# Optimization experiments

Hardware: AMD Instinct MI355X
Metric: run time of the kernel (lower is better)

## Reference

```python
import jax, jax.numpy as jnp
import numpy as np

RELU_SCALE = 0.25  # const power-of-two activation scale for QuantReLU (uint4)
DN = ('NCHW', 'OIHW', 'NCHW')
BN_EPS = 1e-5


def ste_round(x):
    # straight-through-estimator round (brevitas RoundSte)
    return x + jax.lax.stop_gradient(jnp.round(x) - x)


def fq_signed(x, bits):
    # per-tensor symmetric fixed-point fake quant with power-of-two scale
    # (Int8WeightPerTensorFixedPoint / Int8ActPerTensorFixedPoint at bit_width=bits)
    n = 2.0 ** (bits - 1) - 1.0
    m = jnp.maximum(jnp.max(jnp.abs(x)), 1e-8)
    s = jax.lax.stop_gradient(jnp.exp2(jnp.ceil(jnp.log2(m / n))))
    return jnp.clip(ste_round(x / s), -n - 1.0, n) * s


def quant_relu4(x):
    # QuantReLU: uint4, CONST power-of-two scale
    return jnp.clip(ste_round(x / RELU_SCALE), 0.0, 15.0) * RELU_SCALE


def bn(x, g, b, m, v):
    # inference-form BatchNorm2d (running stats)
    inv = g * jax.lax.rsqrt(v + BN_EPS)
    return x * inv[None, :, None, None] + (b - m * inv)[None, :, None, None]


def qconv(x, w, stride, groups):
    # QuantConv2d: fake-quant input (int4) and weight (int4), then conv
    xq = fq_signed(x, 4)
    wq = fq_signed(w, 4)
    pad = 'VALID' if w.shape[-1] == 1 else ((1, 1), (1, 1))
    return jax.lax.conv_general_dilated(
        xq, wq, (stride, stride), pad,
        dimension_numbers=DN, feature_group_count=groups)


def setup_inputs() -> dict:
    key = jax.random.key(0)
    ks = jax.random.split(key, 24)
    B, Cin, H, W = 32, 64, 56, 56
    expansion, Cout = 6, 96
    P = expansion * Cin  # 384

    def bn_params(i, C):
        g = jax.random.uniform(ks[i], (C,), minval=0.5, maxval=1.5)
        b = jax.random.normal(ks[i + 1], (C,)) * 0.1
        m = jax.random.normal(ks[i + 2], (C,)) * 0.1
        v = jax.random.uniform(ks[i + 3], (C,), minval=0.5, maxval=1.5)
        return g, b, m, v

    x = jax.random.normal(ks[0], (B, Cin, H, W), dtype=jnp.float32)
    w1 = jax.random.normal(ks[1], (P, Cin, 1, 1), dtype=jnp.float32) * 0.1
    w2 = jax.random.normal(ks[2], (P, 1, 3, 3), dtype=jnp.float32) * 0.1
    w3 = jax.random.normal(ks[3], (Cout, P, 1, 1), dtype=jnp.float32) * 0.1
    ws = jax.random.normal(ks[4], (Cout, Cin, 1, 1), dtype=jnp.float32) * 0.1
    g1, b1, m1, v1 = bn_params(5, P)
    g2, b2, m2, v2 = bn_params(9, P)
    g3, b3, m3, v3 = bn_params(13, Cout)
    gs, bs, ms, vs = bn_params(17, Cout)
    return {
        'x': x,
        'w1': w1, 'g1': g1, 'b1': b1, 'm1': m1, 'v1': v1,
        'w2': w2, 'g2': g2, 'b2': b2, 'm2': m2, 'v2': v2,
        'w3': w3, 'g3': g3, 'b3': b3, 'm3': m3, 'v3': v3,
        'ws': ws, 'gs': gs, 'bs': bs, 'ms': ms, 'vs': vs,
    }


def reference(x, w1, g1, b1, m1, v1, w2, g2, b2, m2, v2,
              w3, g3, b3, m3, v3, ws, gs, bs, ms, vs):
    P = w1.shape[0]
    # expand 1x1 -> BN -> QuantReLU
    out = quant_relu4(bn(qconv(x, w1, 1, 1), g1, b1, m1, v1))
    # depthwise 3x3 (stride=1) -> BN -> QuantReLU
    out = quant_relu4(bn(qconv(out, w2, 1, P), g2, b2, m2, v2))
    # project 1x1 with int8 output_quant -> BN
    out = bn(fq_signed(qconv(out, w3, 1, 1), 8), g3, b3, m3, v3)
    # shortcut: 1x1 quant conv (int4 output_quant) -> BN  (stride==1, Cin!=Cout)
    sc = bn(fq_signed(qconv(x, ws, 1, 1), 4), gs, bs, ms, vs)
    return quant_relu4(out + sc)
```

## Files before the change

kernel.cpp:

```cpp
#include <hip/hip_runtime.h>
#include <stdint.h>

#define B_  32
#define CIN 64
#define H_  56
#define W_  56
#define HW_ 3136
#define P_  384
#define CO_ 96

typedef unsigned short u16;
typedef short v2s __attribute__((ext_vector_type(2)));

__device__ __forceinline__ v2s as_v2s(int x) {
    union { int i; v2s v; } u; u.i = x; return u.v;
}

__device__ __forceinline__ float pot_scale(float m, float n) {
    float q = fmaxf(m, 1e-8f) / n;
    int e; float f = frexpf(q, &e);
    return ldexpf(1.0f, (f == 0.5f) ? (e - 1) : e);
}

__device__ __forceinline__ int dot8(int a, int b, int c) {
#if __has_builtin(__builtin_amdgcn_sdot8)
    return __builtin_amdgcn_sdot8(a, b, c, false);
#else
#pragma unroll
    for (int j = 0; j < 8; j++) {
        int av = (a << (28 - 4 * j)) >> 28;
        int bv = (b << (28 - 4 * j)) >> 28;
        c += av * bv;
    }
    return c;
#endif
}

__device__ __forceinline__ int iclamp(int v, int lo, int hi) { return min(max(v, lo), hi); }

__device__ __forceinline__ unsigned build_lut(float r, int lo) {
    unsigned v = 0;
#pragma unroll
    for (int L = 0; L < 8; L++)
        v |= (unsigned)min((int)rintf(__fmul_rn((float)(lo + L), r)), 7) << (4 * L);
    return v;
}
__device__ __forceinline__ int lut1(unsigned lo, unsigned hi, int L) {
    unsigned sel = (L & 8) ? hi : lo;
    return (int)((sel >> ((L & 7) * 4)) & 7u);
}

__device__ __forceinline__ int wave_max(int v) {
#pragma unroll
    for (int off = 32; off > 0; off >>= 1) v = max(v, __shfl_xor(v, off, 64));
    return v;
}
__device__ __forceinline__ int block_max_w(int v, int* red, int slot, int nw) {
    v = wave_max(v);
    int wid = threadIdx.x >> 6;
    if ((threadIdx.x & 63) == 0) red[slot * 8 + wid] = v;
    __syncthreads();
    int r = red[slot * 8];
#pragma unroll 4
    for (int i = 1; i < nw; i++) r = max(r, red[slot * 8 + i]);
    return r;
}

#define SMAX_RD(sm, q, dst) { dst = 0; _Pragma("unroll") \
    for (int s_ = 0; s_ < 16; s_++) dst = max(dst, (sm)[(q) * 256 + s_ * 16]); }

__global__ __launch_bounds__(1024) void k_init_bn(
    float* sf, int* smax, float* bnb,
    const float* g1, const float* b1, const float* m1, const float* v1,
    const float* g2, const float* b2, const float* m2, const float* v2,
    const float* g3, const float* b3, const float* m3, const float* v3,
    const float* gs, const float* bs, const float* ms, const float* vs)
{
    int t = threadIdx.x;
    if (t < 32) ((int*)sf)[t] = 0;
    smax[t] = 0;
    if (t < 384) {
        float inv = __fmul_rn(g1[t], __fdiv_rn(1.0f, sqrtf(__fadd_rn(v1[t], 1e-5f))));
        bnb[t] = inv;
        bnb[384 + t] = __fsub_rn(b1[t], __fmul_rn(m1[t], inv));
    } else if (t < 768) {
        int i = t - 384;
        float inv = __fmul_rn(g2[i], __fdiv_rn(1.0f, sqrtf(__fadd_rn(v2[i], 1e-5f))));
        bnb[768 + i] = inv;
        bnb[1152 + i] = __fsub_rn(b2[i], __fmul_rn(m2[i], inv));
    } else if (t < 864) {
        int i = t - 768;
        float inv = __fmul_rn(g3[i], __fdiv_rn(1.0f, sqrtf(__fadd_rn(v3[i], 1e-5f))));
        bnb[1536 + i] = inv;
        bnb[1632 + i] = __fsub_rn(b3[i], __fmul_rn(m3[i], inv));
    } else if (t < 960) {
        int i = t - 864;
        float inv = __fmul_rn(gs[i], __fdiv_rn(1.0f, sqrtf(__fadd_rn(vs[i], 1e-5f))));
        bnb[1728 + i] = inv;
        bnb[1824 + i] = __fsub_rn(bs[i], __fmul_rn(ms[i], inv));
    }
}

#define XBLK 384
__global__ __launch_bounds__(256) void k_maxes(
    const float* __restrict__ x, const float* __restrict__ w1,
    const float* __restrict__ w2, const float* __restrict__ w3,
    const float* __restrict__ wsc, float* sf)
{
    __shared__ int red[16];
    int tid = threadIdx.x;
    float m = 0.f;
    if (blockIdx.x < XBLK) {
        const float4* x4 = (const float4*)x;
        const int n4 = (B_ * CIN * HW_) / 4;
        for (int i = blockIdx.x * 256 + tid; i < n4; i += XBLK * 256) {
            float4 v = x4[i];
            m = fmaxf(m, fmaxf(fmaxf(fabsf(v.x), fabsf(v.y)),
                               fmaxf(fabsf(v.z), fabsf(v.w))));
        }
        int bm = block_max_w(__float_as_int(m), red, 0, 4);
        if (tid == 0) atomicMax((int*)&sf[0], bm);
    } else {
        int seg = blockIdx.x - XBLK;
        const float* p = seg == 0 ? w1 : seg == 1 ? w2 : seg == 2 ? w3 : wsc;
        int n = seg == 0 ? P_ * CIN : seg == 1 ? P_ * 9 : seg == 2 ? CO_ * P_ : CO_ * CIN;
        for (int i = tid; i < n; i += 256) m = fmaxf(m, fabsf(p[i]));
        int bm = block_max_w(__float_as_int(m), red, 0, 4);
        if (tid == 0) atomicMax((int*)&sf[1 + seg], bm);
    }
}

__global__ __launch_bounds__(256) void k_quantw(
    const float* __restrict__ w1, const float* __restrict__ w2,
    const float* __restrict__ w3, const float* __restrict__ wsc,
    const float* __restrict__ sf,
    int* __restrict__ w1n, int8_t* __restrict__ w2q,
    int* __restrict__ w3n, int* __restrict__ wsn)
{
    int flat = blockIdx.x * 256 + threadIdx.x;
    if (flat < 3072) {
        int d = flat, co = d & 3, k8 = (d >> 2) & 7, g = d >> 5;
        float r = 1.0f / pot_scale(sf[1], 7.f);
        const float* src = w1 + (4 * g + co) * 64 + 8 * k8;
        unsigned pk = 0;
#pragma unroll
        for (int j = 0; j < 8; j++) {
            int q = iclamp((int)rintf(__fmul_rn(src[j], r)), -8, 7);
            pk |= (unsigned)(q & 0xF) << (4 * j);
        }
        w1n[d] = (int)pk;
    } else if (flat < 7680) {
        int d = flat - 3072, co = d & 3, k8 = (d >> 2) % 48, coq = d / 192;
        float r = 1.0f / pot_scale(sf[3], 7.f);
        const float* src = w3 + (4 * coq + co) * 384 + 8 * k8;
        unsigned pk = 0;
#pragma unroll
        for (int j = 0; j < 8; j++) {
            int q = iclamp((int)rintf(__fmul_rn(src[j], r)), -8, 7);
            pk |= (unsigned)(q & 0xF) << (4 * j);
        }
        w3n[d] = (int)pk;
    } else if (flat < 8448) {
        int d = flat - 7680, co = d & 3, k8 = (d >> 2) & 7, coq = d >> 5;
        float r = 1.0f / pot_scale(sf[4], 7.f);
        const float* src = wsc + (4 * coq + co) * 64 + 8 * k8;
        unsigned pk = 0;
#pragma unroll
        for (int j = 0; j < 8; j++) {
            int q = iclamp((int)rintf(__fmul_rn(src[j], r)), -8, 7);
            pk |= (unsigned)(q & 0xF) << (4 * j);
        }
        wsn[d] = (int)pk;
    } else if (flat < 11904) {
        int i = flat - 8448;
        float r = 1.0f / pot_scale(sf[2], 7.f);
        w2q[i] = (int8_t)iclamp((int)rintf(__fmul_rn(w2[i], r)), -8, 7);
    }
}

__global__ __launch_bounds__(192) void k_conv1(
    const float* __restrict__ x, const int4* __restrict__ w1n,
    const int4* __restrict__ wsn,
    const float* __restrict__ sf, const float* __restrict__ bnb,
    u16* __restrict__ out1h, int* __restrict__ xq4, int* smax)
{
    __shared__ __align__(16) int xs[8 * W_];
    __shared__ __align__(16) u16 otile[96 * W_];
    __shared__ int red[16];
    int tid = threadIdx.x;
    int b = blockIdx.x / H_, h = blockIdx.x % H_;
    float rx = 1.0f / pot_scale(sf[0], 7.0f);
    for (int i = tid; i < 8 * W_; i += 192) {
        int c8 = i / W_, w = i % W_;
        const float* xp = x + (size_t)(b * 64 + c8 * 8) * HW_ + h * W_ + w;
        unsigned pk = 0;
#pragma unroll
        for (int j = 0; j < 8; j++) {
            int q = iclamp((int)rintf(__fmul_rn(xp[(size_t)j * HW_], rx)), -8, 7);
            pk |= (unsigned)(q & 0xF) << (4 * j);
        }
        xs[i] = (int)pk;
        xq4[(size_t)(b * 8 + c8) * HW_ + h * W_ + w] = (int)pk;
    }
    float sprod = __fmul_rn(pot_scale(sf[0], 7.f), pot_scale(sf[1], 7.f));
    __syncthreads();
    int g = tid % 96, half = tid / 96;
    int4 wreg[8];
    {
        const int4* wp = w1n + g * 8;
#pragma unroll
        for (int k = 0; k < 8; k++) wreg[k] = wp[k];
    }
    float4 invv = *(const float4*)&bnb[4 * g];
    float4 betv = *(const float4*)&bnb[384 + 4 * g];
    float inva[4] = {invv.x, invv.y, invv.z, invv.w};
    float beta[4] = {betv.x, betv.y, betv.z, betv.w};
    int lmax = 0;
#pragma unroll
    for (int q = 0; q < 7; q++) {
        int w4 = half * 28 + q * 4;
        int acc[4][4];
#pragma unroll
        for (int c = 0; c < 4; c++)
#pragma unroll
            for (int w = 0; w < 4; w++) acc[c][w] = 0;
#pragma unroll
        for (int k = 0; k < 8; k++) {
            int4 wv = wreg[k];
            int4 xv = *(const int4*)&xs[k * W_ + w4];
            acc[0][0] = dot8(xv.x, wv.x, acc[0][0]); acc[0][1] = dot8(xv.y, wv.x, acc[0][1]);
            acc[0][2] = dot8(xv.z, wv.x, acc[0][2]); acc[0][3] = dot8(xv.w, wv.x, acc[0][3]);
            acc[1][0] = dot8(xv.x, wv.y, acc[1][0]); acc[1][1] = dot8(xv.y, wv.y, acc[1][1]);
            acc[1][2] = dot8(xv.z, wv.y, acc[1][2]); acc[1][3] = dot8(xv.w, wv.y, acc[1][3]);
            acc[2][0] = dot8(xv.x, wv.z, acc[2][0]); acc[2][1] = dot8(xv.y, wv.z, acc[2][1]);
            acc[2][2] = dot8(xv.z, wv.z, acc[2][2]); acc[2][3] = dot8(xv.w, wv.z, acc[2][3]);
            acc[3][0] = dot8(xv.x, wv.w, acc[3][0]); acc[3][1] = dot8(xv.y, wv.w, acc[3][1]);
            acc[3][2] = dot8(xv.z, wv.w, acc[3][2]); acc[3][3] = dot8(xv.w, wv.w, acc[3][3]);
        }
        unsigned lv[4];
#pragma unroll
        for (int w = 0; w < 4; w++) {
            unsigned pkd = 0;
#pragma unroll
            for (int c = 0; c < 4; c++) {
                float y = __fadd_rn(__fmul_rn(__fmul_rn((float)acc[c][w], sprod), inva[c]), beta[c]);
                int L = iclamp((int)rintf(__fmul_rn(y, 4.f)), 0, 15);
                lmax = max(lmax, L);
                pkd |= (unsigned)L << (4 * c);
            }
            lv[w] = pkd;
        }
        *(uint2*)&otile[g * W_ + w4] =
            make_uint2(lv[0] | (lv[1] << 16), lv[2] | (lv[3] << 16));
    }
    __syncthreads();
    {
        u16* baseo = out1h + (size_t)(b * 96) * HW_ + h * W_;
        for (int i = tid; i < 96 * 7; i += 192) {
            int gg = i / 7, wq = (i % 7) * 8;
            *(uint4*)(baseo + (size_t)gg * HW_ + wq) = *(uint4*)&otile[gg * W_ + wq];
        }
    }
    int bm = block_max_w(lmax, red, 0, 3);
    if (tid == 0) atomicMax(&smax[0 * 256 + (blockIdx.x & 15) * 16], bm);
    int amax = 0;
    for (int qi = tid; qi < 336; qi += 192) {
        int coq = qi / 14, w4 = (qi % 14) * 4;
        int acc[4][4];
#pragma unroll
        for (int c = 0; c < 4; c++)
#pragma unroll
            for (int w = 0; w < 4; w++) acc[c][w] = 0;
        const int4* wp = wsn + coq * 8;
#pragma unroll
        for (int k = 0; k < 8; k++) {
            int4 wv = wp[k];
            int4 xv = *(const int4*)&xs[k * W_ + w4];
            acc[0][0] = dot8(xv.x, wv.x, acc[0][0]); acc[0][1] = dot8(xv.y, wv.x, acc[0][1]);
            acc[0][2] = dot8(xv.z, wv.x, acc[0][2]); acc[0][3] = dot8(xv.w, wv.x, acc[0][3]);
            acc[1][0] = dot8(xv.x, wv.y, acc[1][0]); acc[1][1] = dot8(xv.y, wv.y, acc[1][1]);
            acc[1][2] = dot8(xv.z, wv.y, acc[1][2]); acc[1][3] = dot8(xv.w, wv.y, acc[1][3]);
            acc[2][0] = dot8(xv.x, wv.z, acc[2][0]); acc[2][1] = dot8(xv.y, wv.z, acc[2][1]);
            acc[2][2] = dot8(xv.z, wv.z, acc[2][2]); acc[2][3] = dot8(xv.w, wv.z, acc[2][3]);
            acc[3][0] = dot8(xv.x, wv.w, acc[3][0]); acc[3][1] = dot8(xv.y, wv.w, acc[3][1]);
            acc[3][2] = dot8(xv.z, wv.w, acc[3][2]); acc[3][3] = dot8(xv.w, wv.w, acc[3][3]);
        }
#pragma unroll
        for (int c = 0; c < 4; c++)
            amax = max(amax, max(max(abs(acc[c][0]), abs(acc[c][1])),
                                 max(abs(acc[c][2]), abs(acc[c][3]))));
    }
    bm = block_max_w(amax, red, 1, 3);
    if (tid == 0) atomicMax(&smax[3 * 256 + (blockIdx.x & 15) * 16], bm);
}

__global__ __launch_bounds__(256) void k_conv2(
    const u16* __restrict__ out1h, const int8_t* __restrict__ w2q,
    const float* __restrict__ sf, int* smax,
    const float* __restrict__ bnb, u16* __restrict__ out2h)
{
    __shared__ int blut[256];
    __shared__ __align__(8) int plane2[58 * 58 * 2];
    __shared__ int red[16];
    int tid = threadIdx.x;
    int b = blockIdx.x / 96, g = blockIdx.x % 96;
    int mL1; SMAX_RD(smax, 0, mL1);
    float s_a2 = pot_scale(0.25f * (float)mL1, 7.f);
    float r2 = 0.25f / s_a2;
    float sprod = __fmul_rn(s_a2, pot_scale(sf[2], 7.f));
    unsigned lutlo = build_lut(r2, 0), luthi = build_lut(r2, 8);
    blut[tid] = (lut1(lutlo, luthi, tid & 0xF) & 0xFFFF)
              | (lut1(lutlo, luthi, tid >> 4) << 16);
    int wv[4][9];
#pragma unroll
    for (int c = 0; c < 4; c++)
#pragma unroll
        for (int t = 0; t < 9; t++) wv[c][t] = (int)w2q[(4 * g + c) * 9 + t];
    int wpk[2][9];
#pragma unroll
    for (int p = 0; p < 2; p++)
#pragma unroll
        for (int t = 0; t < 9; t++)
            wpk[p][t] = (wv[2 * p][t] & 0xFFFF) | (wv[2 * p + 1][t] << 16);
    float4 invv = *(const float4*)&bnb[768 + 4 * g];
    float4 betv = *(const float4*)&bnb[1152 + 4 * g];
    float inva[4] = {invv.x, invv.y, invv.z, invv.w};
    float beta[4] = {betv.x, betv.y, betv.z, betv.w};
    __syncthreads();
    const u16* src = out1h + (size_t)(b * 96 + g) * HW_;
    for (int i = tid; i < 58 * 58; i += 256) {
        int r = i / 58, c = i % 58;
        int pv0 = 0, pv1 = 0;
        if (r >= 1 && r <= 56 && c >= 1 && c <= 56) {
            unsigned v = src[(r - 1) * W_ + (c - 1)];
            pv0 = blut[v & 0xFFu];
            pv1 = blut[(v >> 8) & 0xFFu];
        }
        *(int2*)&plane2[2 * i] = make_int2(pv0, pv1);
    }
    __syncthreads();
    int lmax = 0;
    int ow = tid & 63, seg = tid >> 6;
    if (ow < 56) {
        int oh0 = seg * 14;
        const int2* pl = (const int2*)plane2;
        u16* dst = out2h + (size_t)(b * 96 + g) * HW_ + ow;
        int2 p00 = pl[oh0 * 58 + ow],       p01 = pl[oh0 * 58 + ow + 1],       p02 = pl[oh0 * 58 + ow + 2];
        int2 p10 = pl[(oh0 + 1) * 58 + ow], p11 = pl[(oh0 + 1) * 58 + ow + 1], p12 = pl[(oh0 + 1) * 58 + ow + 2];
#pragma unroll 2
        for (int oh = oh0; oh < oh0 + 14; oh++) {
            int2 p20 = pl[(oh + 2) * 58 + ow], p21 = pl[(oh + 2) * 58 + ow + 1],
                 p22 = pl[(oh + 2) * 58 + ow + 2];
            v2s a0 = as_v2s(p00.x) * as_v2s(wpk[0][0]);
            a0 += as_v2s(p01.x) * as_v2s(wpk[0][1]);
            a0 += as_v2s(p02.x) * as_v2s(wpk[0][2]);
            a0 += as_v2s(p10.x) * as_v2s(wpk[0][3]);
            a0 += as_v2s(p11.x) * as_v2s(wpk[0][4]);
            a0 += as_v2s(p12.x) * as_v2s(wpk[0][5]);
            a0 += as_v2s(p20.x) * as_v2s(wpk[0][6]);
            a0 += as_v2s(p21.x) * as_v2s(wpk[0][7]);
            a0 += as_v2s(p22.x) * as_v2s(wpk[0][8]);
            v2s a1 = as_v2s(p00.y) * as_v2s(wpk[1][0]);
            a1 += as_v2s(p01.y) * as_v2s(wpk[1][1]);
            a1 += as_v2s(p02.y) * as_v2s(wpk[1][2]);
            a1 += as_v2s(p10.y) * as_v2s(wpk[1][3]);
            a1 += as_v2s(p11.y) * as_v2s(wpk[1][4]);
            a1 += as_v2s(p12.y) * as_v2s(wpk[1][5]);
            a1 += as_v2s(p20.y) * as_v2s(wpk[1][6]);
            a1 += as_v2s(p21.y) * as_v2s(wpk[1][7]);
            a1 += as_v2s(p22.y) * as_v2s(wpk[1][8]);
            int acca[4] = {(int)a0.x, (int)a0.y, (int)a1.x, (int)a1.y};
            unsigned pkd = 0;
#pragma unroll
            for (int c = 0; c < 4; c++) {
                float y = __fadd_rn(__fmul_rn(__fmul_rn((float)acca[c], sprod), inva[c]), beta[c]);
                int L = iclamp((int)rintf(__fmul_rn(y, 4.f)), 0, 15);
                lmax = max(lmax, L);
                pkd |= (unsigned)L << (4 * c);
            }
            dst[oh * W_] = (u16)pkd;
            p00 = p10; p01 = p11; p02 = p12;
            p10 = p20; p11 = p21; p12 = p22;
        }
    }
    int bm = block_max_w(lmax, red, 0, 4);
    if (tid == 0) atomicMax(&smax[1 * 256 + (blockIdx.x & 15) * 16], bm);
}

__global__ __launch_bounds__(256) void k_conv3(
    const u16* __restrict__ out2h, const int4* __restrict__ w3n,
    const float* __restrict__ sf, int* smax,
    int16_t* __restrict__ acc3)
{
    __shared__ __align__(16) int a3s[2 * 48 * W_];
    __shared__ int nlut[256];
    __shared__ int red[16];
    int tid = threadIdx.x;
    int b = blockIdx.x / 28, h0 = (blockIdx.x % 28) * 2;
    int mL2; SMAX_RD(smax, 1, mL2);
    float s_a3 = pot_scale(0.25f * (float)mL2, 7.f);
    float r3 = 0.25f / s_a3;
    unsigned lutlo = build_lut(r3, 0), luthi = build_lut(r3, 8);
    nlut[tid] = lut1(lutlo, luthi, tid & 0xF) | (lut1(lutlo, luthi, tid >> 4) << 4);
    __syncthreads();
    for (int i = tid; i < 2 * 48 * W_; i += 256) {
        int row = i / (48 * W_), rem = i % (48 * W_), c8 = rem / W_, w = rem % W_;
        size_t base = (size_t)(b * 96 + c8 * 2) * HW_ + (h0 + row) * W_ + w;
        unsigned v0 = out2h[base], v1 = out2h[base + HW_];
        unsigned q0 = (unsigned)nlut[v0 & 0xFFu] | ((unsigned)nlut[(v0 >> 8) & 0xFFu] << 8);
        unsigned q1 = (unsigned)nlut[v1 & 0xFFu] | ((unsigned)nlut[(v1 >> 8) & 0xFFu] << 8);
        a3s[i] = (int)(q0 | (q1 << 16));
    }
    __syncthreads();
    int amax = 0;
    for (int qi = tid; qi < 672; qi += 256) {
        int coq = qi / 28, rem2 = qi % 28, row = rem2 / 14, w4 = (rem2 % 14) * 4;
        int acc[4][4];
#pragma unroll
        for (int c = 0; c < 4; c++)
#pragma unroll
            for (int w = 0; w < 4; w++) acc[c][w] = 0;
        const int4* wp = w3n + coq * 48;
        const int* ap = a3s + row * 48 * W_ + w4;
#pragma unroll 6
        for (int k = 0; k < 48; k++) {
            int4 wv = wp[k];
            int4 av = *(const int4*)(ap + k * W_);
            acc[0][0] = dot8(av.x, wv.x, acc[0][0]); acc[0][1] = dot8(av.y, wv.x, acc[0][1]);
            acc[0][2] = dot8(av.z, wv.x, acc[0][2]); acc[0][3] = dot8(av.w, wv.x, acc[0][3]);
            acc[1][0] = dot8(av.x, wv.y, acc[1][0]); acc[1][1] = dot8(av.y, wv.y, acc[1][1]);
            acc[1][2] = dot8(av.z, wv.y, acc[1][2]); acc[1][3] = dot8(av.w, wv.y, acc[1][3]);
            acc[2][0] = dot8(av.x, wv.z, acc[2][0]); acc[2][1] = dot8(av.y, wv.z, acc[2][1]);
            acc[2][2] = dot8(av.z, wv.z, acc[2][2]); acc[2][3] = dot8(av.w, wv.z, acc[2][3]);
            acc[3][0] = dot8(av.x, wv.w, acc[3][0]); acc[3][1] = dot8(av.y, wv.w, acc[3][1]);
            acc[3][2] = dot8(av.z, wv.w, acc[3][2]); acc[3][3] = dot8(av.w, wv.w, acc[3][3]);
        }
#pragma unroll
        for (int c = 0; c < 4; c++) {
            int co = coq * 4 + c;
            amax = max(amax, max(max(abs(acc[c][0]), abs(acc[c][1])),
                                 max(abs(acc[c][2]), abs(acc[c][3]))));
            short4 st = make_short4((short)acc[c][0], (short)acc[c][1],
                                    (short)acc[c][2], (short)acc[c][3]);
            *(short4*)(acc3 + (size_t)(b * CO_ + co) * HW_ + (h0 + row) * W_ + w4) = st;
        }
    }
    int bm = block_max_w(amax, red, 0, 4);
    if (tid == 0) atomicMax(&smax[2 * 256 + (blockIdx.x & 15) * 16], bm);
}

__global__ __launch_bounds__(256) void k_final(
    const int* __restrict__ xq4, const int4* __restrict__ wsn,
    const int16_t* __restrict__ acc3, const float* __restrict__ sf,
    const int* __restrict__ smax, const float* __restrict__ bnb,
    float* __restrict__ dout)
{
    __shared__ __align__(16) int xs[8 * W_];
    int tid = threadIdx.x;
    int b = blockIdx.x / H_, h = blockIdx.x % H_;
    for (int i = tid; i < 8 * W_; i += 256)
        xs[i] = xq4[((b * 8 + i / W_) * HW_) + h * W_ + (i % W_)];
    int mL2, mA3, mAS;
    SMAX_RD(smax, 1, mL2); SMAX_RD(smax, 2, mA3); SMAX_RD(smax, 3, mAS);
    float s_a3   = pot_scale(0.25f * (float)mL2, 7.f);
    float sprod3 = __fmul_rn(s_a3, pot_scale(sf[3], 7.f));
    float s_q3   = pot_scale(__fmul_rn(sprod3, (float)mA3), 127.f);
    float rq3    = sprod3 / s_q3;
    float sprods = __fmul_rn(pot_scale(sf[0], 7.f), pot_scale(sf[4], 7.f));
    float s_qs   = pot_scale(__fmul_rn(sprods, (float)mAS), 7.f);
    float rqs    = sprods / s_qs;
    __syncthreads();
    for (int qi = tid; qi < 24 * 14; qi += 256) {
        int coq = qi / 14, w4 = (qi % 14) * 4;
        int acc[4][4];
#pragma unroll
        for (int c = 0; c < 4; c++)
#pragma unroll
            for (int w = 0; w < 4; w++) acc[c][w] = 0;
        const int4* wp = wsn + coq * 8;
#pragma unroll
        for (int k = 0; k < 8; k++) {
            int4 wv = wp[k];
            int4 xv = *(const int4*)&xs[k * W_ + w4];
            acc[0][0] = dot8(xv.x, wv.x, acc[0][0]); acc[0][1] = dot8(xv.y, wv.x, acc[0][1]);
            acc[0][2] = dot8(xv.z, wv.x, acc[0][2]); acc[0][3] = dot8(xv.w, wv.x, acc[0][3]);
            acc[1][0] = dot8(xv.x, wv.y, acc[1][0]); acc[1][1] = dot8(xv.y, wv.y, acc[1][1]);
            acc[1][2] = dot8(xv.z, wv.y, acc[1][2]); acc[1][3] = dot8(xv.w, wv.y, acc[1][3]);
            acc[2][0] = dot8(xv.x, wv.z, acc[2][0]); acc[2][1] = dot8(xv.y, wv.z, acc[2][1]);
            acc[2][2] = dot8(xv.z, wv.z, acc[2][2]); acc[2][3] = dot8(xv.w, wv.z, acc[2][3]);
            acc[3][0] = dot8(xv.x, wv.w, acc[3][0]); acc[3][1] = dot8(xv.y, wv.w, acc[3][1]);
            acc[3][2] = dot8(xv.z, wv.w, acc[3][2]); acc[3][3] = dot8(xv.w, wv.w, acc[3][3]);
        }
        float4 inv3v = *(const float4*)&bnb[1536 + 4 * coq];
        float4 bet3v = *(const float4*)&bnb[1632 + 4 * coq];
        float4 invSv = *(const float4*)&bnb[1728 + 4 * coq];
        float4 betSv = *(const float4*)&bnb[1824 + 4 * coq];
        float inv3a[4] = {inv3v.x, inv3v.y, inv3v.z, inv3v.w};
        float bet3a[4] = {bet3v.x, bet3v.y, bet3v.z, bet3v.w};
        float invSa[4] = {invSv.x, invSv.y, invSv.z, invSv.w};
        float betSa[4] = {betSv.x, betSv.y, betSv.z, betSv.w};
#pragma unroll
        for (int c = 0; c < 4; c++) {
            int co = coq * 4 + c;
            size_t idx = (size_t)(b * CO_ + co) * HW_ + h * W_ + w4;
            short4 c3 = *(const short4*)(acc3 + idx);
            int c3a[4] = {c3.x, c3.y, c3.z, c3.w};
            float4 o4;
            float* o = (float*)&o4;
#pragma unroll
            for (int j = 0; j < 4; j++) {
                int q3 = iclamp((int)rintf(__fmul_rn((float)c3a[j], rq3)), -128, 127);
                float y3 = __fadd_rn(__fmul_rn(__fmul_rn((float)q3, s_q3), inv3a[c]), bet3a[c]);
                int qs = iclamp((int)rintf(__fmul_rn((float)acc[c][j], rqs)), -8, 7);
                float ys = __fadd_rn(__fmul_rn(__fmul_rn((float)qs, s_qs), invSa[c]), betSa[c]);
                float oo = __fadd_rn(y3, ys);
                int L = iclamp((int)rintf(__fmul_rn(oo, 4.f)), 0, 15);
                o[j] = (float)L * 0.25f;
            }
            *(float4*)(dout + idx) = o4;
        }
    }
}

extern "C" void kernel_launch(void* const* d_in, const int* in_sizes, int n_in,
                              void* d_out, int out_size, void* d_ws, size_t ws_size,
                              hipStream_t stream)
{
    const float* x   = (const float*)d_in[0];
    const float* w1  = (const float*)d_in[1];
    const float* g1  = (const float*)d_in[2];
    const float* b1  = (const float*)d_in[3];
    const float* m1  = (const float*)d_in[4];
    const float* v1  = (const float*)d_in[5];
    const float* w2  = (const float*)d_in[6];
    const float* g2  = (const float*)d_in[7];
    const float* b2  = (const float*)d_in[8];
    const float* m2  = (const float*)d_in[9];
    const float* v2  = (const float*)d_in[10];
    const float* w3  = (const float*)d_in[11];
    const float* g3  = (const float*)d_in[12];
    const float* b3  = (const float*)d_in[13];
    const float* m3  = (const float*)d_in[14];
    const float* v3  = (const float*)d_in[15];
    const float* wsc = (const float*)d_in[16];
    const float* gs  = (const float*)d_in[17];
    const float* bs  = (const float*)d_in[18];
    const float* ms  = (const float*)d_in[19];
    const float* vs  = (const float*)d_in[20];

    char* ws = (char*)d_ws;
    float*   sf    = (float*)ws;
    float*   bnb   = (float*)(ws + 256);
    int*     w1n   = (int*)(ws + 8192);
    int8_t*  w2q   = (int8_t*)(ws + 32768);
    int*     w3n   = (int*)(ws + 36864);
    int*     wsn   = (int*)(ws + 73728);
    int*     smax  = (int*)(ws + 102400);
    int*     xq4   = (int*)(ws + (1u << 20));
    u16*     out1h = (u16*)(ws + (8u << 20));
    int16_t* acc3  = (int16_t*)(ws + (8u << 20));
    u16*     out2h = (u16*)(ws + (48u << 20));

    k_init_bn<<<1, 1024, 0, stream>>>(sf, smax, bnb, g1, b1, m1, v1, g2, b2, m2, v2,
                                      g3, b3, m3, v3, gs, bs, ms, vs);
    k_maxes<<<XBLK + 4, 256, 0, stream>>>(x, w1, w2, w3, wsc, sf);
    k_quantw<<<47, 256, 0, stream>>>(w1, w2, w3, wsc, sf, w1n, w2q, w3n, wsn);
    k_conv1<<<B_ * H_, 192, 0, stream>>>(x, (const int4*)w1n, (const int4*)wsn,
                                         sf, bnb, out1h, xq4, smax);
    k_conv2<<<B_ * 96, 256, 0, stream>>>(out1h, w2q, sf, smax, bnb, out2h);
    k_conv3<<<B_ * 28, 256, 0, stream>>>(out2h, (const int4*)w3n, sf, smax, acc3);
    k_final<<<B_ * H_, 256, 0, stream>>>(xq4, (const int4*)wsn, acc3, sf, smax, bnb,
                                         (float*)d_out);
}
```

Before: 261.7 us.

## Process two rows per conv1 block, vectorize x loads, fold BN init into maxes

k_conv1 now handles two output rows per block, so each block reuses its register-held expand weights over twice the pixels and the grid halves. The input quantization loop reads float4 vectors and writes int4 packs instead of scalars. The separate BN-init kernel is removed: its work runs in extra blocks of k_maxes, and the max buffers are zeroed with memset calls. This cuts launch overhead and per-block weight loading, at the cost of larger shared memory per block and fewer blocks for latency hiding.

```diff
diff --git a/kernel.cpp b/kernel.cpp
--- a/kernel.cpp
+++ b/kernel.cpp
@@ -69,46 +69,42 @@
 #define SMAX_RD(sm, q, dst) { dst = 0; _Pragma("unroll") \
     for (int s_ = 0; s_ < 16; s_++) dst = max(dst, (sm)[(q) * 256 + s_ * 16]); }
 
-__global__ __launch_bounds__(1024) void k_init_bn(
-    float* sf, int* smax, float* bnb,
+#define XBLK 384
+__global__ __launch_bounds__(256) void k_maxes(
+    const float* __restrict__ x, const float* __restrict__ w1,
+    const float* __restrict__ w2, const float* __restrict__ w3,
+    const float* __restrict__ wsc, float* sf, float* bnb,
     const float* g1, const float* b1, const float* m1, const float* v1,
     const float* g2, const float* b2, const float* m2, const float* v2,
     const float* g3, const float* b3, const float* m3, const float* v3,
     const float* gs, const float* bs, const float* ms, const float* vs)
 {
-    int t = threadIdx.x;
-    if (t < 32) ((int*)sf)[t] = 0;
-    smax[t] = 0;
-    if (t < 384) {
-        float inv = __fmul_rn(g1[t], __fdiv_rn(1.0f, sqrtf(__fadd_rn(v1[t], 1e-5f))));
-        bnb[t] = inv;
-        bnb[384 + t] = __fsub_rn(b1[t], __fmul_rn(m1[t], inv));
-    } else if (t < 768) {
-        int i = t - 384;
-        float inv = __fmul_rn(g2[i], __fdiv_rn(1.0f, sqrtf(__fadd_rn(v2[i], 1e-5f))));
-        bnb[768 + i] = inv;
-        bnb[1152 + i] = __fsub_rn(b2[i], __fmul_rn(m2[i], inv));
-    } else if (t < 864) {
-        int i = t - 768;
-        float inv = __fmul_rn(g3[i], __fdiv_rn(1.0f, sqrtf(__fadd_rn(v3[i], 1e-5f))));
-        bnb[1536 + i] = inv;
-        bnb[1632 + i] = __fsub_rn(b3[i], __fmul_rn(m3[i], inv));
-    } else if (t < 960) {
-        int i = t - 864;
-        float inv = __fmul_rn(gs[i], __fdiv_rn(1.0f, sqrtf(__fadd_rn(vs[i], 1e-5f))));
-        bnb[1728 + i] = inv;
-        bnb[1824 + i] = __fsub_rn(bs[i], __fmul_rn(ms[i], inv));
-    }
-}
-
-#define XBLK 384
-__global__ __launch_bounds__(256) void k_maxes(
-    const float* __restrict__ x, const float* __restrict__ w1,
-    const float* __restrict__ w2, const float* __restrict__ w3,
-    const float* __restrict__ wsc, float* sf)
-{
     __shared__ int red[16];
     int tid = threadIdx.x;
+    if (blockIdx.x >= XBLK + 4) {
+        int t = (blockIdx.x - XBLK - 4) * 256 + tid;
+        if (t < 384) {
+            float inv = __fmul_rn(g1[t], __fdiv_rn(1.0f, sqrtf(__fadd_rn(v1[t], 1e-5f))));
+            bnb[t] = inv;
+            bnb[384 + t] = __fsub_rn(b1[t], __fmul_rn(m1[t], inv));
+        } else if (t < 768) {
+            int i = t - 384;
+            float inv = __fmul_rn(g2[i], __fdiv_rn(1.0f, sqrtf(__fadd_rn(v2[i], 1e-5f))));
+            bnb[768 + i] = inv;
+            bnb[1152 + i] = __fsub_rn(b2[i], __fmul_rn(m2[i], inv));
+        } else if (t < 864) {
+            int i = t - 768;
+            float inv = __fmul_rn(g3[i], __fdiv_rn(1.0f, sqrtf(__fadd_rn(v3[i], 1e-5f))));
+            bnb[1536 + i] = inv;
+            bnb[1632 + i] = __fsub_rn(b3[i], __fmul_rn(m3[i], inv));
+        } else if (t < 960) {
+            int i = t - 864;
+            float inv = __fmul_rn(gs[i], __fdiv_rn(1.0f, sqrtf(__fadd_rn(vs[i], 1e-5f))));
+            bnb[1728 + i] = inv;
+            bnb[1824 + i] = __fsub_rn(bs[i], __fmul_rn(ms[i], inv));
+        }
+        return;
+    }
     float m = 0.f;
     if (blockIdx.x < XBLK) {
         const float4* x4 = (const float4*)x;
@@ -184,23 +180,29 @@
     const float* __restrict__ sf, const float* __restrict__ bnb,
     u16* __restrict__ out1h, int* __restrict__ xq4, int* smax)
 {
-    __shared__ __align__(16) int xs[8 * W_];
-    __shared__ __align__(16) u16 otile[96 * W_];
+    __shared__ __align__(16) int xs[2 * 8 * W_];
+    __shared__ __align__(16) u16 otile[2 * 96 * W_];
     __shared__ int red[16];
     int tid = threadIdx.x;
-    int b = blockIdx.x / H_, h = blockIdx.x % H_;
+    int b = blockIdx.x / 28, h0 = (blockIdx.x % 28) * 2;
     float rx = 1.0f / pot_scale(sf[0], 7.0f);
-    for (int i = tid; i < 8 * W_; i += 192) {
-        int c8 = i / W_, w = i % W_;
-        const float* xp = x + (size_t)(b * 64 + c8 * 8) * HW_ + h * W_ + w;
-        unsigned pk = 0;
+    for (int i = tid; i < 224; i += 192) {
+        int row = i / 112, rem = i % 112, c8 = rem / 14, w4 = (rem % 14) * 4;
+        const float* xp = x + (size_t)(b * 64 + c8 * 8) * HW_ + (h0 + row) * W_ + w4;
+        unsigned pk[4] = {0, 0, 0, 0};
 #pragma unroll
         for (int j = 0; j < 8; j++) {
-            int q = iclamp((int)rintf(__fmul_rn(xp[(size_t)j * HW_], rx)), -8, 7);
-            pk |= (unsigned)(q & 0xF) << (4 * j);
-        }
-        xs[i] = (int)pk;
-        xq4[(size_t)(b * 8 + c8) * HW_ + h * W_ + w] = (int)pk;
+            float4 v = *(const float4*)(xp + (size_t)j * HW_);
+            float va[4] = {v.x, v.y, v.z, v.w};
+#pragma unroll
+            for (int w = 0; w < 4; w++) {
+                int q = iclamp((int)rintf(__fmul_rn(va[w], rx)), -8, 7);
+                pk[w] |= (unsigned)(q & 0xF) << (4 * j);
+            }
+        }
+        int4 st = make_int4((int)pk[0], (int)pk[1], (int)pk[2], (int)pk[3]);
+        *(int4*)&xs[row * 8 * W_ + c8 * W_ + w4] = st;
+        *(int4*)(xq4 + (size_t)(b * 8 + c8) * HW_ + (h0 + row) * W_ + w4) = st;
     }
     float sprod = __fmul_rn(pot_scale(sf[0], 7.f), pot_scale(sf[1], 7.f));
     __syncthreads();
@@ -217,55 +219,61 @@
     float beta[4] = {betv.x, betv.y, betv.z, betv.w};
     int lmax = 0;
 #pragma unroll
-    for (int q = 0; q < 7; q++) {
-        int w4 = half * 28 + q * 4;
-        int acc[4][4];
-#pragma unroll
-        for (int c = 0; c < 4; c++)
-#pragma unroll
-            for (int w = 0; w < 4; w++) acc[c][w] = 0;
-#pragma unroll
-        for (int k = 0; k < 8; k++) {
-            int4 wv = wreg[k];
-            int4 xv = *(const int4*)&xs[k * W_ + w4];
-            acc[0][0] = dot8(xv.x, wv.x, acc[0][0]); acc[0][1] = dot8(xv.y, wv.x, acc[0][1]);
-            acc[0][2] = dot8(xv.z, wv.x, acc[0][2]); acc[0][3] = dot8(xv.w, wv.x, acc[0][3]);
-            acc[1][0] = dot8(xv.x, wv.y, acc[1][0]); acc[1][1] = dot8(xv.y, wv.y, acc[1][1]);
-            acc[1][2] = dot8(xv.z, wv.y, acc[1][2]); acc[1][3] = dot8(xv.w, wv.y, acc[1][3]);
-            acc[2][0] = dot8(xv.x, wv.z, acc[2][0]); acc[2][1] = dot8(xv.y, wv.z, acc[2][1]);
-            acc[2][2] = dot8(xv.z, wv.z, acc[2][2]); acc[2][3] = dot8(xv.w, wv.z, acc[2][3]);
-            acc[3][0] = dot8(xv.x, wv.w, acc[3][0]); acc[3][1] = dot8(xv.y, wv.w, acc[3][1]);
-            acc[3][2] = dot8(xv.z, wv.w, acc[3][2]); acc[3][3] = dot8(xv.w, wv.w, acc[3][3]);
-        }
-        unsigned lv[4];
-#pragma unroll
-        for (int w = 0; w < 4; w++) {
-            unsigned pkd = 0;
-#pragma unroll
-            for (int c = 0; c < 4; c++) {
-                float y = __fadd_rn(__fmul_rn(__fmul_rn((float)acc[c][w], sprod), inva[c]), beta[c]);
-                int L = iclamp((int)rintf(__fmul_rn(y, 4.f)), 0, 15);
-                lmax = max(lmax, L);
-                pkd |= (unsigned)L << (4 * c);
+    for (int row = 0; row < 2; row++) {
+        const int* xrow = xs + row * 8 * W_;
+        u16* orow = otile + row * 96 * W_;
+#pragma unroll
+        for (int q = 0; q < 7; q++) {
+            int w4 = half * 28 + q * 4;
+            int acc[4][4];
+#pragma unroll
+            for (int c = 0; c < 4; c++)
+#pragma unroll
+                for (int w = 0; w < 4; w++) acc[c][w] = 0;
+#pragma unroll
+            for (int k = 0; k < 8; k++) {
+                int4 wv = wreg[k];
+                int4 xv = *(const int4*)&xrow[k * W_ + w4];
+                acc[0][0] = dot8(xv.x, wv.x, acc[0][0]); acc[0][1] = dot8(xv.y, wv.x, acc[0][1]);
+                acc[0][2] = dot8(xv.z, wv.x, acc[0][2]); acc[0][3] = dot8(xv.w, wv.x, acc[0][3]);
+                acc[1][0] = dot8(xv.x, wv.y, acc[1][0]); acc[1][1] = dot8(xv.y, wv.y, acc[1][1]);
+                acc[1][2] = dot8(xv.z, wv.y, acc[1][2]); acc[1][3] = dot8(xv.w, wv.y, acc[1][3]);
+                acc[2][0] = dot8(xv.x, wv.z, acc[2][0]); acc[2][1] = dot8(xv.y, wv.z, acc[2][1]);
+                acc[2][2] = dot8(xv.z, wv.z, acc[2][2]); acc[2][3] = dot8(xv.w, wv.z, acc[2][3]);
+                acc[3][0] = dot8(xv.x, wv.w, acc[3][0]); acc[3][1] = dot8(xv.y, wv.w, acc[3][1]);
+                acc[3][2] = dot8(xv.z, wv.w, acc[3][2]); acc[3][3] = dot8(xv.w, wv.w, acc[3][3]);
             }
-            lv[w] = pkd;
-        }
-        *(uint2*)&otile[g * W_ + w4] =
-            make_uint2(lv[0] | (lv[1] << 16), lv[2] | (lv[3] << 16));
+            unsigned lv[4];
+#pragma unroll
+            for (int w = 0; w < 4; w++) {
+                unsigned pkd = 0;
+#pragma unroll
+                for (int c = 0; c < 4; c++) {
+                    float y = __fadd_rn(__fmul_rn(__fmul_rn((float)acc[c][w], sprod), inva[c]), beta[c]);
+                    int L = iclamp((int)rintf(__fmul_rn(y, 4.f)), 0, 15);
+                    lmax = max(lmax, L);
+                    pkd |= (unsigned)L << (4 * c);
+                }
+                lv[w] = pkd;
+            }
+            *(uint2*)&orow[g * W_ + w4] =
+                make_uint2(lv[0] | (lv[1] << 16), lv[2] | (lv[3] << 16));
+        }
     }
     __syncthreads();
     {
-        u16* baseo = out1h + (size_t)(b * 96) * HW_ + h * W_;
-        for (int i = tid; i < 96 * 7; i += 192) {
-            int gg = i / 7, wq = (i % 7) * 8;
-            *(uint4*)(baseo + (size_t)gg * HW_ + wq) = *(uint4*)&otile[gg * W_ + wq];
+        for (int i = tid; i < 2 * 96 * 7; i += 192) {
+            int row = i / 672, rem = i % 672, gg = rem / 7, wq = (rem % 7) * 8;
+            *(uint4*)(out1h + (size_t)(b * 96 + gg) * HW_ + (h0 + row) * W_ + wq) =
+                *(uint4*)&otile[row * 96 * W_ + gg * W_ + wq];
         }
     }
     int bm = block_max_w(lmax, red, 0, 3);
     if (tid == 0) atomicMax(&smax[0 * 256 + (blockIdx.x & 15) * 16], bm);
     int amax = 0;
-    for (int qi = tid; qi < 336; qi += 192) {
-        int coq = qi / 14, w4 = (qi % 14) * 4;
+    for (int qi = tid; qi < 672; qi += 192) {
+        int row = qi / 336, rem = qi % 336, coq = rem / 14, w4 = (rem % 14) * 4;
+        const int* xrow = xs + row * 8 * W_;
         int acc[4][4];
 #pragma unroll
         for (int c = 0; c < 4; c++)
@@ -275,7 +283,7 @@
 #pragma unroll
         for (int k = 0; k < 8; k++) {
             int4 wv = wp[k];
-            int4 xv = *(const int4*)&xs[k * W_ + w4];
+            int4 xv = *(const int4*)&xrow[k * W_ + w4];
             acc[0][0] = dot8(xv.x, wv.x, acc[0][0]); acc[0][1] = dot8(xv.y, wv.x, acc[0][1]);
             acc[0][2] = dot8(xv.z, wv.x, acc[0][2]); acc[0][3] = dot8(xv.w, wv.x, acc[0][3]);
             acc[1][0] = dot8(xv.x, wv.y, acc[1][0]); acc[1][1] = dot8(xv.y, wv.y, acc[1][1]);
@@ -561,11 +569,13 @@
     int16_t* acc3  = (int16_t*)(ws + (8u << 20));
     u16*     out2h = (u16*)(ws + (48u << 20));
 
-    k_init_bn<<<1, 1024, 0, stream>>>(sf, smax, bnb, g1, b1, m1, v1, g2, b2, m2, v2,
-                                      g3, b3, m3, v3, gs, bs, ms, vs);
-    k_maxes<<<XBLK + 4, 256, 0, stream>>>(x, w1, w2, w3, wsc, sf);
+    hipMemsetAsync(sf, 0, 256, stream);
+    hipMemsetAsync(smax, 0, 4096, stream);
+    k_maxes<<<XBLK + 8, 256, 0, stream>>>(x, w1, w2, w3, wsc, sf, bnb,
+                                          g1, b1, m1, v1, g2, b2, m2, v2,
+                                          g3, b3, m3, v3, gs, bs, ms, vs);
     k_quantw<<<47, 256, 0, stream>>>(w1, w2, w3, wsc, sf, w1n, w2q, w3n, wsn);
-    k_conv1<<<B_ * H_, 192, 0, stream>>>(x, (const int4*)w1n, (const int4*)wsn,
+    k_conv1<<<B_ * 28, 192, 0, stream>>>(x, (const int4*)w1n, (const int4*)wsn,
                                          sf, bnb, out1h, xq4, smax);
     k_conv2<<<B_ * 96, 256, 0, stream>>>(out1h, w2q, sf, smax, bnb, out2h);
     k_conv3<<<B_ * 28, 256, 0, stream>>>(out2h, (const int4*)w3n, sf, smax, acc3);
```

Measured after the change: 269.9 us. 1.03x slower.
